# Kernel optimization log

Hardware: AMD Instinct MI355X
Metric: run time of the kernel (lower is better)

## Reference

```python
import jax, jax.numpy as jnp
import numpy as np

# SLAY feature-map hyperparams (must match init_kwargs)
H, D, P, M, R = 4, 128, 16, 32, 2   # heads, head_dim, poly_dim, num_features, quad nodes
EPS = 1e-6
C = 2.0 + EPS
_nodes, _weights = np.polynomial.laguerre.laggauss(R)
QUAD_NODES = jnp.asarray(_nodes, jnp.float32) / C
QUAD_WEIGHTS = jnp.asarray(_weights, jnp.float32) / C

VOCAB, NUM_LABELS, EMBED_DIM = 100000, 32768, 512
B, S, K = 512, 64, 5


def slay_features(x, omega, anchors):
    """SLAY feature map: tensor product of anchored polynomial and PRF features.
    x: [N, EMBED_DIM] -> [N, R*H*P*M]"""
    N = x.shape[0]
    xr = x.reshape(N, H, D)
    xn = xr / jnp.clip(jnp.linalg.norm(xr, axis=-1, keepdims=True), 1e-6)  # safe_normalize
    # anchored polynomial features: [N, H, P]
    poly_feat = jnp.einsum('nhd,pd->nhp', xn, anchors) ** 2 / jnp.sqrt(float(P))
    # positive random features with Gauss-Laguerre quadrature: [R, N, H, M]
    prf_proj = jnp.einsum('nhd,rhdm->rnhm', xn, omega)
    s = QUAD_NODES.reshape(R, 1, 1, 1)
    sqrt_2s = jnp.sqrt(2.0 * jnp.clip(s, 0))
    prf_feat = jnp.exp(jnp.clip(prf_proj * sqrt_2s - s, -10.0, 10.0)) / jnp.sqrt(float(M))
    prf_feat = prf_feat * jnp.sqrt(jnp.clip(QUAD_WEIGHTS.reshape(R, 1, 1, 1), 0))
    # tensor-product fusion: [N, R, H, P, M] -> [N, R*H*P*M]
    fused = jnp.einsum('nhp,rnhm->nrhpm', poly_feat, prf_feat)
    return fused.reshape(N, -1)


def mean_embedding(indices, mask, embedding_table):
    embeds = embedding_table[indices]                       # [B, S, E]
    sum_embeds = jnp.sum(embeds * mask[:, :, None], axis=1)  # [B, E]
    sum_mask = jnp.sum(mask, axis=1, keepdims=True)
    return sum_embeds / jnp.clip(sum_mask, 1e-9)


def setup_inputs() -> dict:
    key = jax.random.key(0)
    k1, k2, k3, k4, k5, k6 = jax.random.split(key, 6)
    indices = jax.random.randint(k1, (B, S), 0, VOCAB)
    mask = jnp.ones((B, S), dtype=jnp.float32)
    labels = jax.random.randint(k2, (B, K), 0, NUM_LABELS)
    label_mask = jnp.ones((B, K), dtype=jnp.float32)
    embedding_table = jax.random.normal(k3, (VOCAB, EMBED_DIM), dtype=jnp.float32) * 0.02
    classifier_kernel = jax.random.normal(k4, (EMBED_DIM, NUM_LABELS), dtype=jnp.float32) * 0.02
    omega = jax.random.normal(k5, (R, H, D, M), dtype=jnp.float32)
    anchors = jax.random.normal(k6, (P, D), dtype=jnp.float32)
    anchors = anchors / jnp.linalg.norm(anchors, axis=-1, keepdims=True)
    return {"indices": indices, "mask": mask, "labels": labels, "label_mask": label_mask,
            "embedding_table": embedding_table, "classifier_kernel": classifier_kernel,
            "omega": omega, "anchors": anchors}


def reference(indices, mask, labels, label_mask, embedding_table, classifier_kernel, omega, anchors):
    query = mean_embedding(indices, mask, embedding_table)            # [B, E]
    phi_query = slay_features(query, omega, anchors)                  # [B, F]
    W_vecs = classifier_kernel.T                                      # [L, E]
    phi_W = slay_features(W_vecs, omega, anchors)                     # [L, F]  (dominant cost)
    Z_approx_vec = jnp.sum(phi_W, axis=0)                             # [F]
    denom = jnp.dot(phi_query, Z_approx_vec) + 1e-6                   # [B]
    log_Z = jnp.log(denom)
    safe_labels = jnp.maximum(labels, 0)
    W_pos = W_vecs[safe_labels]                                       # [B, K, E]
    phi_w_pos = slay_features(W_pos.reshape(-1, EMBED_DIM), omega, anchors).reshape(B, K, -1)
    nums = jnp.sum(phi_w_pos * phi_query[:, None, :], axis=-1) + 1e-6  # [B, K]
    log_probs = jnp.log(nums) - log_Z[:, None]
    loss_total = -jnp.sum(log_probs * label_mask)
    return loss_total / B
```

## Files before the change

### kernel.cpp

```cpp
#include <hip/hip_runtime.h>
#include <math.h>


namespace {
constexpr double Cq  = 2.0 + 1e-6;
constexpr double QN0 = 0.5857864376269049  / Cq;
constexpr double QN1 = 3.414213562373095   / Cq;
constexpr double QW0 = 0.8535533905932738  / Cq;
constexpr double QW1 = 0.14644660940672624 / Cq;

constexpr size_t OFF_POLYQ = 0;
constexpr size_t OFF_PRFQ  = 32768;
constexpr size_t OFF_Z     = OFF_PRFQ + 131072;
constexpr size_t OFF_ANCT  = OFF_Z + 4096;
constexpr size_t OFF_SLOT  = OFF_ANCT + 2048;
constexpr size_t OFF_FEAT  = OFF_SLOT + 32768;
constexpr size_t OFF_WPACK = OFF_FEAT + 819200;
constexpr size_t OFF_ZPART = OFF_WPACK + 43008;
}

__global__ void k_setup_a(const float* __restrict__ anchors,
                          const float* __restrict__ omega,
                          int* __restrict__ slot, float* __restrict__ Z,
                          float* __restrict__ out, float* __restrict__ anct,
                          float* __restrict__ Wpack)
{
    int t = blockIdx.x * 256 + threadIdx.x;
    for (int i = t; i < 32768; i += 16384) slot[i] = -1;
    if (t < 4096) Z[t] = 0.f;
    if (t == 0) out[0] = 0.f;
    if (t < 2048) {
        int p = t & 15, d = t >> 4;
        anct[t] = anchors[p * 128 + d];
    }
    for (int i = t; i < 4 * 128 * 84; i += 16384) {
        int o = i % 84, hd = i / 84, d = hd & 127, h = hd >> 7;
        float v = 0.f;
        if (o < 16) v = anchors[o * 128 + d];
        else if (o < 80) {
            int r = (o - 16) >> 5, m = (o - 16) & 31;
            v = omega[(((r * 4 + h) * 128) + d) * 32 + m];
        }
        Wpack[i] = v;
    }
}

__global__ void k_setup_b(const int* __restrict__ labels, int* __restrict__ slot)
{
    int i = blockIdx.x * 256 + threadIdx.x;
    if (i < 2560) slot[max(labels[i], 0)] = i;
}

__global__ void __launch_bounds__(256) k_embed_feat(const int* __restrict__ idx,
        const float* __restrict__ mask, const float* __restrict__ emb,
        const float* __restrict__ anct, const float* __restrict__ omega,
        float* __restrict__ polyq, float* __restrict__ prfq)
{
    __shared__ float xs[512];
    __shared__ float rnS[4];
    int b = blockIdx.x, t = threadIdx.x;

    float2 acc = make_float2(0.f, 0.f);
    float msum = 0.f;
#pragma unroll 8
    for (int s = 0; s < 64; ++s) {
        float mv = mask[b * 64 + s];
        const float2* row = (const float2*)(emb + (size_t)idx[b * 64 + s] * 512);
        float2 v = row[t];
        acc.x = fmaf(mv, v.x, acc.x);
        acc.y = fmaf(mv, v.y, acc.y);
        msum += mv;
    }
    float inv = 1.0f / fmaxf(msum, 1e-9f);
    xs[2 * t]     = acc.x * inv;
    xs[2 * t + 1] = acc.y * inv;
    __syncthreads();

    int w = t >> 6, lane = t & 63;
    {
        float v0 = xs[w * 128 + lane], v1 = xs[w * 128 + 64 + lane];
        float ss = fmaf(v0, v0, v1 * v1);
#pragma unroll
        for (int o = 1; o < 64; o <<= 1) ss += __shfl_xor(ss, o, 64);
        if (lane == 0) rnS[w] = 1.0f / fmaxf(sqrtf(ss), 1e-6f);
    }
    __syncthreads();

    const float s_[2] = {(float)QN0, (float)QN1};
    const float g_[2] = {sqrtf(2.0f * (float)QN0), sqrtf(2.0f * (float)QN1)};
    const float c_[2] = {sqrtf((float)QW0) * 0.17677669529663687f,
                         sqrtf((float)QW1) * 0.17677669529663687f};

    for (int tau = t; tau < 320; tau += 256) {
        int h = tau / 80, j = tau - h * 80;
        const float* xh = xs + h * 128;
        float a = 0.f;
        if (j < 16) {
            for (int d = 0; d < 128; ++d) a = fmaf(xh[d], anct[d * 16 + j], a);
            float v = a * rnS[h];
            polyq[(b * 4 + h) * 16 + j] = v * v * 0.25f;
        } else {
            int rj = j - 16, r = rj >> 5, m = rj & 31;
            const float* om = omega + ((size_t)(r * 4 + h) * 128) * 32 + m;
            for (int d = 0; d < 128; ++d) a = fmaf(xh[d], om[d * 32], a);
            float z = a * rnS[h] * g_[r] - s_[r];
            z = fminf(fmaxf(z, -10.f), 10.f);
            prfq[((b * 2 + r) * 4 + h) * 32 + m] = expf(z) * c_[r];
        }
    }
}

__global__ void __launch_bounds__(256) k_labels(const float* __restrict__ ck,
                                                const float* __restrict__ Wpack,
                                                const int* __restrict__ slot,
                                                float* __restrict__ feat,
                                                float* __restrict__ Zpart)
{
    __shared__ float xs[8192];
    __shared__ int slS[64];
    float* ex = xs;

    int t = threadIdx.x, w = t >> 6, lane = t & 63;
    int bid = blockIdx.x;
    int g = bid >> 2, h = bid & 3;
    int l0 = g * 64;

    if (t < 64) slS[t] = slot[l0 + t];

    {
        const float* src = ck + (size_t)h * 128 * 32768 + l0;
#pragma unroll
        for (int k = 0; k < 32; ++k) {
            int idx = k * 256 + t;
            int d = idx >> 6, lab = idx & 63;
            xs[idx] = src[(size_t)d * 32768 + lab];
        }
    }
    __syncthreads();

    int o0u = __builtin_amdgcn_readfirstlane(w * 21);
    const float* wrow = Wpack + (size_t)h * 128 * 84 + o0u;
    float acc[21] = {};
    float sumsq = 0.f;
    for (int d = 0; d < 128; ++d) {
        float xv = xs[d * 64 + lane];
        sumsq = fmaf(xv, xv, sumsq);
        const float* c = wrow + d * 84;
#pragma unroll
        for (int i = 0; i < 21; ++i) acc[i] = fmaf(xv, c[i], acc[i]);
    }
    __syncthreads();

#pragma unroll
    for (int i = 0; i < 21; ++i) {
        int o = o0u + i;
        if (o < 80) ex[lane * 85 + o] = acc[i];
    }
    if (w == 3) ex[lane * 85 + 80] = sumsq;
    __syncthreads();

    {
        int l = t & 63, part = t >> 6, o0 = part * 20;
        float rn = 1.0f / fmaxf(sqrtf(ex[l * 85 + 80]), 1e-6f);
        const float s_[2] = {(float)QN0, (float)QN1};
        const float g_[2] = {sqrtf(2.0f * (float)QN0), sqrtf(2.0f * (float)QN1)};
        const float c_[2] = {sqrtf((float)QW0) * 0.17677669529663687f,
                             sqrtf((float)QW1) * 0.17677669529663687f};
#pragma unroll
        for (int i = 0; i < 20; ++i) {
            int o = o0 + i;
            float v = ex[l * 85 + o];
            if (o < 16) {
                v = v * rn;
                v = v * v * 0.25f;
            } else {
                int r = (o - 16) >> 5;
                float z = v * rn * g_[r] - s_[r];
                z = fminf(fmaxf(z, -10.f), 10.f);
                v = expf(z) * c_[r];
            }
            ex[l * 85 + o] = v;
        }
    }
    __syncthreads();

    for (int j = 0; j < 64; ++j) {
        int s = slS[j];
        if (s >= 0 && t < 80)
            feat[((size_t)s * 4 + h) * 80 + t] = ex[j * 85 + t];
    }

    if (t < 128) {
        int r = t >> 6, p0 = ((t >> 3) & 7) * 2, m0 = (t & 7) * 4;
        float z0[4] = {}, z1[4] = {};
        for (int j = 0; j < 64; ++j) {
            const float* row = ex + j * 85;
            float pa = row[p0], pb = row[p0 + 1];
            const float* pf = row + 16 + r * 32 + m0;
#pragma unroll
            for (int k = 0; k < 4; ++k) {
                float fv = pf[k];
                z0[k] = fmaf(pa, fv, z0[k]);
                z1[k] = fmaf(pb, fv, z1[k]);
            }
        }
        float* zp = Zpart + (size_t)bid * 1024;
#pragma unroll
        for (int k = 0; k < 4; ++k) {
            zp[(r * 16 + p0) * 32 + m0 + k]     = z0[k];
            zp[(r * 16 + p0 + 1) * 32 + m0 + k] = z1[k];
        }
    }
}

__global__ void k_zreduce(const float* __restrict__ Zpart, float* __restrict__ Z)
{
    int tid = blockIdx.x * 256 + threadIdx.x;
    int e = tid & 1023, h = (tid >> 10) & 3, chunk = tid >> 12;
    float sum = 0.f;
    int g0 = chunk * 64;
#pragma unroll 4
    for (int g = g0; g < g0 + 64; ++g)
        sum += Zpart[(size_t)((g << 2) | h) * 1024 + e];
    atomicAdd(&Z[(e >> 9) * 2048 + h * 512 + (e & 511)], sum);
}

__global__ void k_final(const float* __restrict__ polyq, const float* __restrict__ prfq,
                        const float* __restrict__ Z, const int* __restrict__ labels,
                        const float* __restrict__ lmask, const int* __restrict__ slot,
                        const float* __restrict__ feat, float* __restrict__ out)
{
    int t = threadIdx.x, lane = t & 63;
    int b = blockIdx.x * 4 + (t >> 6);

    float acc = 0.f;
    for (int i = 0; i < 64; ++i) {
        int f = i * 64 + lane;
        int m = f & 31, p = (f >> 5) & 15, hh = (f >> 9) & 3, r = f >> 11;
        float phi = polyq[(b * 4 + hh) * 16 + p] * prfq[((b * 2 + r) * 4 + hh) * 32 + m];
        acc = fmaf(phi, Z[f], acc);
    }
#pragma unroll
    for (int o = 1; o < 64; o <<= 1) acc += __shfl_xor(acc, o, 64);
    float logZb = logf(acc + 1e-6f);

    if (lane < 20) {
        int k = lane >> 2, h = lane & 3;
        int l = max(labels[b * 5 + k], 0);
        int s = slot[l];
        const float4* f4 = (const float4*)(feat + ((size_t)s * 4 + h) * 80);
        const float* pq = polyq + (b * 4 + h) * 16;
        const float* q0 = prfq + ((b * 2 + 0) * 4 + h) * 32;
        const float* q1 = prfq + ((b * 2 + 1) * 4 + h) * 32;

        float pd = 0.f;
#pragma unroll
        for (int j = 0; j < 4; ++j) {
            float4 fp = f4[j];
            pd = fmaf(fp.x, pq[4*j+0], pd);
            pd = fmaf(fp.y, pq[4*j+1], pd);
            pd = fmaf(fp.z, pq[4*j+2], pd);
            pd = fmaf(fp.w, pq[4*j+3], pd);
        }
        float f0 = 0.f, f1 = 0.f;
#pragma unroll
        for (int j = 0; j < 8; ++j) {
            float4 fv = f4[4 + j];
            f0 = fmaf(fv.x, q0[4*j+0], f0);
            f0 = fmaf(fv.y, q0[4*j+1], f0);
            f0 = fmaf(fv.z, q0[4*j+2], f0);
            f0 = fmaf(fv.w, q0[4*j+3], f0);
            float4 fw = f4[12 + j];
            f1 = fmaf(fw.x, q1[4*j+0], f1);
            f1 = fmaf(fw.y, q1[4*j+1], f1);
            f1 = fmaf(fw.z, q1[4*j+2], f1);
            f1 = fmaf(fw.w, q1[4*j+3], f1);
        }
        float c = pd * (f0 + f1);
        c += __shfl_xor(c, 1, 64);
        c += __shfl_xor(c, 2, 64);
        if (h == 0) {
            float val = (logf(c + 1e-6f) - logZb) * lmask[b * 5 + k];
            atomicAdd(out, val * (-1.0f / 512.0f));
        }
    }
}

extern "C" void kernel_launch(void* const* d_in, const int* in_sizes, int n_in,
                              void* d_out, int out_size, void* d_ws, size_t ws_size,
                              hipStream_t stream)
{
    const int*   indices = (const int*)  d_in[0];
    const float* mask    = (const float*)d_in[1];
    const int*   labels  = (const int*)  d_in[2];
    const float* lmask   = (const float*)d_in[3];
    const float* emb     = (const float*)d_in[4];
    const float* ck      = (const float*)d_in[5];
    const float* omega   = (const float*)d_in[6];
    const float* anchors = (const float*)d_in[7];
    float* ws  = (float*)d_ws;
    float* out = (float*)d_out;
    int*   slot = (int*)(ws + OFF_SLOT);

    k_setup_a<<<64, 256, 0, stream>>>(anchors, omega, slot, ws + OFF_Z, out,
                                      ws + OFF_ANCT, ws + OFF_WPACK);
    k_setup_b<<<10, 256, 0, stream>>>(labels, slot);
    k_embed_feat<<<512, 256, 0, stream>>>(indices, mask, emb, ws + OFF_ANCT, omega,
                                          ws + OFF_POLYQ, ws + OFF_PRFQ);
    k_labels<<<2048, 256, 0, stream>>>(ck, ws + OFF_WPACK, slot,
                                       ws + OFF_FEAT, ws + OFF_ZPART);
    k_zreduce<<<128, 256, 0, stream>>>(ws + OFF_ZPART, ws + OFF_Z);
    k_final<<<128, 256, 0, stream>>>(ws + OFF_POLYQ, ws + OFF_PRFQ, ws + OFF_Z,
                                     labels, lmask, slot, ws + OFF_FEAT, out);
}
```

Before: 392.8 us.

## Shrink k_labels LDS, pad Wpack per wave, spread Z partials over all threads

The label-feature kernel now stages the classifier columns in two 64-row halves into a smaller shared buffer, which it reuses for the feature exchange, and sets launch bounds for 6 blocks per CU to raise occupancy. Wpack is re-laid out per wave with rows padded to 24 floats, so each wave reads a contiguous aligned slice. The scatter of label features loops only over set bits of a ballot hit mask. The Z partial accumulation now uses all 256 threads and writes float4 stores. The costs are an extra barrier per half and more register pressure under the tighter launch bound.

```diff
diff --git a/kernel.cpp b/kernel.cpp
--- a/kernel.cpp
+++ b/kernel.cpp
@@ -16,7 +16,7 @@
 constexpr size_t OFF_SLOT  = OFF_ANCT + 2048;
 constexpr size_t OFF_FEAT  = OFF_SLOT + 32768;
 constexpr size_t OFF_WPACK = OFF_FEAT + 819200;
-constexpr size_t OFF_ZPART = OFF_WPACK + 43008;
+constexpr size_t OFF_ZPART = OFF_WPACK + 49152;
 }
 
 __global__ void k_setup_a(const float* __restrict__ anchors,
@@ -33,13 +33,16 @@
         int p = t & 15, d = t >> 4;
         anct[t] = anchors[p * 128 + d];
     }
-    for (int i = t; i < 4 * 128 * 84; i += 16384) {
-        int o = i % 84, hd = i / 84, d = hd & 127, h = hd >> 7;
+    for (int i = t; i < 4 * 4 * 128 * 24; i += 16384) {
+        int c = i % 24, d = (i / 24) & 127, w = (i / (24 * 128)) & 3, h = i / (24 * 128 * 4);
+        int o = w * 21 + c;
         float v = 0.f;
-        if (o < 16) v = anchors[o * 128 + d];
-        else if (o < 80) {
-            int r = (o - 16) >> 5, m = (o - 16) & 31;
-            v = omega[(((r * 4 + h) * 128) + d) * 32 + m];
+        if (c < 21 && o < 80) {
+            if (o < 16) v = anchors[o * 128 + d];
+            else {
+                int r = (o - 16) >> 5, m = (o - 16) & 31;
+                v = omega[(((r * 4 + h) * 128) + d) * 32 + m];
+            }
         }
         Wpack[i] = v;
     }
@@ -110,50 +113,56 @@
     }
 }
 
-__global__ void __launch_bounds__(256) k_labels(const float* __restrict__ ck,
-                                                const float* __restrict__ Wpack,
-                                                const int* __restrict__ slot,
-                                                float* __restrict__ feat,
-                                                float* __restrict__ Zpart)
-{
-    __shared__ float xs[8192];
+__global__ void __launch_bounds__(256, 6) k_labels(const float* __restrict__ ck,
+                                                   const float* __restrict__ Wpack,
+                                                   const int* __restrict__ slot,
+                                                   float* __restrict__ feat,
+                                                   float* __restrict__ Zpart)
+{
+    __shared__ float ex[5440];
     __shared__ int slS[64];
-    float* ex = xs;
+    __shared__ unsigned long long hitmaskS;
 
     int t = threadIdx.x, w = t >> 6, lane = t & 63;
-    int bid = blockIdx.x;
-    int g = bid >> 2, h = bid & 3;
+    int bid = blockIdx.x, g = bid >> 2, h = bid & 3;
     int l0 = g * 64;
 
-    if (t < 64) slS[t] = slot[l0 + t];
-
-    {
-        const float* src = ck + (size_t)h * 128 * 32768 + l0;
-#pragma unroll
-        for (int k = 0; k < 32; ++k) {
-            int idx = k * 256 + t;
-            int d = idx >> 6, lab = idx & 63;
-            xs[idx] = src[(size_t)d * 32768 + lab];
-        }
-    }
-    __syncthreads();
-
-    int o0u = __builtin_amdgcn_readfirstlane(w * 21);
-    const float* wrow = Wpack + (size_t)h * 128 * 84 + o0u;
+    int sl = -1;
+    if (t < 64) { sl = slot[l0 + t]; slS[t] = sl; }
+    if (w == 0) {
+        unsigned long long m = __ballot(sl >= 0);
+        if (lane == 0) hitmaskS = m;
+    }
+
+    const float* src = ck + (size_t)h * 128 * 32768 + l0;
+    const float* wrow = Wpack + ((size_t)h * 4 + w) * 128 * 24;
+
     float acc[21] = {};
     float sumsq = 0.f;
-    for (int d = 0; d < 128; ++d) {
-        float xv = xs[d * 64 + lane];
-        sumsq = fmaf(xv, xv, sumsq);
-        const float* c = wrow + d * 84;
-#pragma unroll
-        for (int i = 0; i < 21; ++i) acc[i] = fmaf(xv, c[i], acc[i]);
+#pragma unroll
+    for (int half = 0; half < 2; ++half) {
+        __syncthreads();
+        const float* s0 = src + (size_t)(half * 64) * 32768;
+#pragma unroll
+        for (int k = 0; k < 16; ++k) {
+            int idx = k * 256 + t;
+            ex[idx] = s0[(size_t)(idx >> 6) * 32768 + (idx & 63)];
+        }
+        __syncthreads();
+        const float* crow = wrow + half * 64 * 24;
+        for (int d = 0; d < 64; ++d) {
+            float xv = ex[d * 64 + lane];
+            sumsq = fmaf(xv, xv, sumsq);
+            const float* c = crow + d * 24;
+#pragma unroll
+            for (int i = 0; i < 21; ++i) acc[i] = fmaf(xv, c[i], acc[i]);
+        }
     }
     __syncthreads();
 
 #pragma unroll
     for (int i = 0; i < 21; ++i) {
-        int o = o0u + i;
+        int o = w * 21 + i;
         if (o < 80) ex[lane * 85 + o] = acc[i];
     }
     if (w == 3) ex[lane * 85 + 80] = sumsq;
@@ -184,32 +193,28 @@
     }
     __syncthreads();
 
-    for (int j = 0; j < 64; ++j) {
+    unsigned long long hits = hitmaskS;
+    while (hits) {
+        int j = __builtin_ctzll(hits);
+        hits &= hits - 1;
         int s = slS[j];
-        if (s >= 0 && t < 80)
-            feat[((size_t)s * 4 + h) * 80 + t] = ex[j * 85 + t];
-    }
-
-    if (t < 128) {
-        int r = t >> 6, p0 = ((t >> 3) & 7) * 2, m0 = (t & 7) * 4;
-        float z0[4] = {}, z1[4] = {};
+        if (t < 80) feat[((size_t)s * 4 + h) * 80 + t] = ex[j * 85 + t];
+    }
+
+    {
+        int r = t >> 7, p = (t >> 3) & 15, m4 = t & 7;
+        float z0 = 0.f, z1 = 0.f, z2 = 0.f, z3 = 0.f;
         for (int j = 0; j < 64; ++j) {
             const float* row = ex + j * 85;
-            float pa = row[p0], pb = row[p0 + 1];
-            const float* pf = row + 16 + r * 32 + m0;
-#pragma unroll
-            for (int k = 0; k < 4; ++k) {
-                float fv = pf[k];
-                z0[k] = fmaf(pa, fv, z0[k]);
-                z1[k] = fmaf(pb, fv, z1[k]);
-            }
-        }
-        float* zp = Zpart + (size_t)bid * 1024;
-#pragma unroll
-        for (int k = 0; k < 4; ++k) {
-            zp[(r * 16 + p0) * 32 + m0 + k]     = z0[k];
-            zp[(r * 16 + p0 + 1) * 32 + m0 + k] = z1[k];
-        }
+            float pv = row[p];
+            const float* pf = row + 16 + r * 32 + m4 * 4;
+            z0 = fmaf(pv, pf[0], z0);
+            z1 = fmaf(pv, pf[1], z1);
+            z2 = fmaf(pv, pf[2], z2);
+            z3 = fmaf(pv, pf[3], z3);
+        }
+        float* zp = Zpart + (size_t)bid * 1024 + (r * 16 + p) * 32 + m4 * 4;
+        *(float4*)zp = make_float4(z0, z1, z2, z3);
     }
 }
 
```

Measured after the change: 522.4 us. 33.0% more time.
